# Kernel optimization log

Hardware: AMD Instinct MI355X
Metric: run time of the kernel (lower is better)

Reference implementation:

```python
import jax, jax.numpy as jnp
import numpy as np

B = 524288

def setup_inputs() -> dict:
    key = jax.random.key(0)
    ks = jax.random.split(key, 9)
    return {
        "x":  jax.random.uniform(ks[0], (B, 1, 9, 9), dtype=jnp.float32),
        "Wc": jax.random.normal(ks[1], (81, 9), dtype=jnp.float32),
        "bc": jax.random.normal(ks[2], (81,), dtype=jnp.float32),
        "Wh": jax.random.normal(ks[3], (27, 9), dtype=jnp.float32),
        "bh": jax.random.normal(ks[4], (27,), dtype=jnp.float32),
        "Wm": jax.random.normal(ks[5], (12, 9), dtype=jnp.float32),
        "bm": jax.random.normal(ks[6], (12,), dtype=jnp.float32),
        "Wo": jax.random.normal(ks[7], (4, 4), dtype=jnp.float32),
        "bo": jax.random.normal(ks[8], (4,), dtype=jnp.float32),
    }

def _forward(x, Wc, bc, Wh, bh, Wm, bm, Wo, bo):
    b = x.shape[0]
    # 9 non-overlapping 3x3 patches (stride 3 over 9x9): (B, 9 patches, 9 pixels)
    p = x[:, 0].reshape(b, 3, 3, 3, 3).transpose(0, 1, 3, 2, 4).reshape(b, 9, 9)
    # conv layer: 9 logic kernels per patch -> (B, 9, 9) -> (B, 81)
    feat = jax.nn.sigmoid(
        jnp.einsum('bgp,gkp->bgk', p, Wc.reshape(9, 9, 9)) + bc.reshape(9, 9)
    ).reshape(b, 81)
    # hidden layer: 9 groups x 3 neurons, each over 9 inputs -> (B, 27)
    h = jax.nn.sigmoid(
        jnp.einsum('bgp,gnp->bgn', feat.reshape(b, 9, 9), Wh.reshape(9, 3, 9))
        + bh.reshape(9, 3)
    ).reshape(b, 27)
    # middle layer: 3 groups x 4 neurons, each over 9 inputs -> (B, 12)
    m = jax.nn.sigmoid(
        jnp.einsum('bgp,gnp->bgn', h.reshape(b, 3, 9), Wm.reshape(3, 4, 9))
        + bm.reshape(3, 4)
    ).reshape(b, 12)
    # output layer: class c reads middle group c % 3 (4 values each)
    num_classes = Wo.shape[0]
    grp = jnp.arange(num_classes) % 3                   # (C,)
    mg = m.reshape(b, 3, 4)[:, grp]                     # (B, C, 4)
    output_logits = jnp.einsum('bcp,cp->bc', mg, Wo) + bo
    return output_logits

def reference(x, Wc, bc, Wh, bh, Wm, bm, Wo, bo):
    return _forward(x, Wc, bc, Wh, bh, Wm, bm, Wo, bo)
```

## Files before the change

### kernel.cpp

```cpp
#include <hip/hip_runtime.h>

#define THREADS 256

__device__ __forceinline__ float fast_sigmoid(float v) {
    float e = __expf(-v);
    return __builtin_amdgcn_rcpf(1.0f + e);
}

__global__ __launch_bounds__(THREADS, 4) void olcnn_kernel(
    const float* __restrict__ x,
    const float* __restrict__ Wc, const float* __restrict__ bc,
    const float* __restrict__ Wh, const float* __restrict__ bh,
    const float* __restrict__ Wm, const float* __restrict__ bm,
    const float* __restrict__ Wo, const float* __restrict__ bo,
    float* __restrict__ out)
{
    const int s = blockIdx.x * THREADS + threadIdx.x;
    const float* xs = x + s * 81;

    float pix[81];
    #pragma unroll
    for (int i = 0; i < 81; ++i) pix[i] = xs[i];

    float res[4];

    #pragma unroll
    for (int G = 0; G < 3; ++G) {
        #pragma unroll
        for (int i = 0; i < 27; ++i) asm volatile("" : "+v"(pix[G * 27 + i]));

        float hbuf[9];
        #pragma unroll
        for (int j = 0; j < 3; ++j) {
            const int g = G * 3 + j;
            float feat[9];
            #pragma unroll
            for (int k = 0; k < 9; ++k) {
                float acc = bc[g * 9 + k];
                #pragma unroll
                for (int pr = 0; pr < 3; ++pr)
                    #pragma unroll
                    for (int pc = 0; pc < 3; ++pc)
                        acc = fmaf(pix[G * 27 + pr * 9 + j * 3 + pc],
                                   Wc[(g * 9 + k) * 9 + pr * 3 + pc], acc);
                feat[k] = fast_sigmoid(acc);
            }
            #pragma unroll
            for (int n = 0; n < 3; ++n) {
                float acc = bh[g * 3 + n];
                #pragma unroll
                for (int p = 0; p < 9; ++p)
                    acc = fmaf(feat[p], Wh[(g * 3 + n) * 9 + p], acc);
                hbuf[j * 3 + n] = fast_sigmoid(acc);
            }
        }

        float m[4];
        #pragma unroll
        for (int n = 0; n < 4; ++n) {
            float acc = bm[G * 4 + n];
            #pragma unroll
            for (int p = 0; p < 9; ++p)
                acc = fmaf(hbuf[p], Wm[(G * 4 + n) * 9 + p], acc);
            m[n] = fast_sigmoid(acc);
        }

        {
            float acc = bo[G];
            #pragma unroll
            for (int p = 0; p < 4; ++p)
                acc = fmaf(m[p], Wo[G * 4 + p], acc);
            res[G] = acc;
        }
        if (G == 0) {
            float acc = bo[3];
            #pragma unroll
            for (int p = 0; p < 4; ++p)
                acc = fmaf(m[p], Wo[3 * 4 + p], acc);
            res[3] = acc;
        }
    }

    float4 o;
    o.x = res[0]; o.y = res[1]; o.z = res[2]; o.w = res[3];
    ((float4*)out)[s] = o;
}

extern "C" void kernel_launch(void* const* d_in, const int* in_sizes, int n_in,
                              void* d_out, int out_size, void* d_ws, size_t ws_size,
                              hipStream_t stream) {
    const float* x  = (const float*)d_in[0];
    const float* Wc = (const float*)d_in[1];
    const float* bc = (const float*)d_in[2];
    const float* Wh = (const float*)d_in[3];
    const float* bh = (const float*)d_in[4];
    const float* Wm = (const float*)d_in[5];
    const float* bm = (const float*)d_in[6];
    const float* Wo = (const float*)d_in[7];
    const float* bo = (const float*)d_in[8];
    float* out = (float*)d_out;

    const int B = in_sizes[0] / 81;
    const int blocks = B / THREADS;
    olcnn_kernel<<<blocks, THREADS, 0, stream>>>(x, Wc, bc, Wh, bh, Wm, bm,
                                                 Wo, bo, out);
}
```

Before: 272.3 us.

## Stage input tile into LDS via coalesced global_load_lds with padded rows

Replaces per-thread strided 81-float loads with cooperative 16-byte global_load_lds transfers that place each sample's row in LDS padded to 84 floats. Each thread then reads its three 27-pixel groups with float4 LDS loads. Block size drops to 64 threads to match the tile, with special handling for the final sample's tail. The goal is coalesced global reads and lower register pressure from not holding all 81 pixels at once, at the cost of LDS usage, a barrier and more complex index math.

```diff
diff --git a/kernel.cpp b/kernel.cpp
--- a/kernel.cpp
+++ b/kernel.cpp
@@ -1,13 +1,19 @@
 #include <hip/hip_runtime.h>
+#include <stdint.h>
 
-#define THREADS 256
+#define THREADS 64
+#define ROWPAD  84
+#define TILE_DW (64 * 81)
+
+typedef const __attribute__((address_space(1))) uint32_t* gas_ptr;
+typedef __attribute__((address_space(3))) uint32_t*       las_ptr;
 
 __device__ __forceinline__ float fast_sigmoid(float v) {
     float e = __expf(-v);
     return __builtin_amdgcn_rcpf(1.0f + e);
 }
 
-__global__ __launch_bounds__(THREADS, 4) void olcnn_kernel(
+__global__ __launch_bounds__(THREADS, 2) void olcnn_kernel(
     const float* __restrict__ x,
     const float* __restrict__ Wc, const float* __restrict__ bc,
     const float* __restrict__ Wh, const float* __restrict__ bh,
@@ -15,19 +21,46 @@
     const float* __restrict__ Wo, const float* __restrict__ bo,
     float* __restrict__ out)
 {
-    const int s = blockIdx.x * THREADS + threadIdx.x;
-    const float* xs = x + s * 81;
+    __shared__ __align__(16) float sm[64 * ROWPAD];
 
-    float pix[81];
-    #pragma unroll
-    for (int i = 0; i < 81; ++i) pix[i] = xs[i];
+    const int lane  = threadIdx.x;
+    const int s     = blockIdx.x * THREADS + lane;
+    const int Wd    = blockIdx.x * TILE_DW;
+    const int TOTAL = (int)gridDim.x * TILE_DW;
+
+    {
+        int t = (lane * 6242) >> 17;
+        int r = lane - t * 21;
+        #pragma unroll
+        for (int i = 0; i < 21; ++i) {
+            const int grp = (r * 19) >> 7;
+            int f0 = Wd + t * 81 + (r << 2) - grp;
+            const int lim = TOTAL - 4;
+            f0 = (f0 < lim) ? f0 : lim;
+            __builtin_amdgcn_global_load_lds(
+                (gas_ptr)(x + f0), (las_ptr)(&sm[i * 256]), 16, 0, 0);
+            t += 3 + (r == 20);
+            r = (r == 20) ? 0 : r + 1;
+        }
+    }
+    __syncthreads();
 
     float res[4];
 
     #pragma unroll
     for (int G = 0; G < 3; ++G) {
-        #pragma unroll
-        for (int i = 0; i < 27; ++i) asm volatile("" : "+v"(pix[G * 27 + i]));
+        float p[28];
+        {
+            const float4* rp = (const float4*)&sm[lane * ROWPAD + G * 28];
+            #pragma unroll
+            for (int q = 0; q < 7; ++q) {
+                float4 v = rp[q];
+                p[4*q+0] = v.x; p[4*q+1] = v.y; p[4*q+2] = v.z; p[4*q+3] = v.w;
+            }
+        }
+        if (G == 2 && blockIdx.x == gridDim.x - 1 && lane == 63) {
+            p[24] = x[TOTAL - 3]; p[25] = x[TOTAL - 2]; p[26] = x[TOTAL - 1];
+        }
 
         float hbuf[9];
         #pragma unroll
@@ -41,7 +74,7 @@
                 for (int pr = 0; pr < 3; ++pr)
                     #pragma unroll
                     for (int pc = 0; pc < 3; ++pc)
-                        acc = fmaf(pix[G * 27 + pr * 9 + j * 3 + pc],
+                        acc = fmaf(p[pr * 9 + j * 3 + pc],
                                    Wc[(g * 9 + k) * 9 + pr * 3 + pc], acc);
                 feat[k] = fast_sigmoid(acc);
             }
@@ -49,8 +82,8 @@
             for (int n = 0; n < 3; ++n) {
                 float acc = bh[g * 3 + n];
                 #pragma unroll
-                for (int p = 0; p < 9; ++p)
-                    acc = fmaf(feat[p], Wh[(g * 3 + n) * 9 + p], acc);
+                for (int pidx = 0; pidx < 9; ++pidx)
+                    acc = fmaf(feat[pidx], Wh[(g * 3 + n) * 9 + pidx], acc);
                 hbuf[j * 3 + n] = fast_sigmoid(acc);
             }
         }
@@ -60,23 +93,23 @@
         for (int n = 0; n < 4; ++n) {
             float acc = bm[G * 4 + n];
             #pragma unroll
-            for (int p = 0; p < 9; ++p)
-                acc = fmaf(hbuf[p], Wm[(G * 4 + n) * 9 + p], acc);
+            for (int pidx = 0; pidx < 9; ++pidx)
+                acc = fmaf(hbuf[pidx], Wm[(G * 4 + n) * 9 + pidx], acc);
             m[n] = fast_sigmoid(acc);
         }
 
         {
             float acc = bo[G];
             #pragma unroll
-            for (int p = 0; p < 4; ++p)
-                acc = fmaf(m[p], Wo[G * 4 + p], acc);
+            for (int pidx = 0; pidx < 4; ++pidx)
+                acc = fmaf(m[pidx], Wo[G * 4 + pidx], acc);
             res[G] = acc;
         }
         if (G == 0) {
             float acc = bo[3];
             #pragma unroll
-            for (int p = 0; p < 4; ++p)
-                acc = fmaf(m[p], Wo[3 * 4 + p], acc);
+            for (int pidx = 0; pidx < 4; ++pidx)
+                acc = fmaf(m[pidx], Wo[3 * 4 + pidx], acc);
             res[3] = acc;
         }
     }
```

New measurement: 306.7 us. 12.6% more time.

## Stage input rows through LDS with async global_load_lds per wave

Applied to the files above, without the earlier changes.

Each thread used to load its own 81 floats with strided per-thread global loads, which coalesce poorly. Now each wave copies one third of its 64 samples' pixels at a time (27 floats padded to 28) into shared memory with 16-byte global_load_lds transfers, then every thread reads its rows back as float4 from LDS. Accesses are clamped at the end of the buffer, and the last sample patches in its final three pixels by hand. The aim is coalesced global traffic and fewer live registers, at the cost of 28 KB of LDS per block and a full vmcnt wait per group with no overlap.

```diff
diff --git a/kernel.cpp b/kernel.cpp
--- a/kernel.cpp
+++ b/kernel.cpp
@@ -1,6 +1,12 @@
 #include <hip/hip_runtime.h>
+#include <stdint.h>
 
 #define THREADS 256
+#define WAVE_DW 1792
+#define GDW     28
+
+typedef const __attribute__((address_space(1))) uint32_t* gas_ptr;
+typedef __attribute__((address_space(3))) uint32_t*       las_ptr;
 
 __device__ __forceinline__ float fast_sigmoid(float v) {
     float e = __expf(-v);
@@ -15,19 +21,54 @@
     const float* __restrict__ Wo, const float* __restrict__ bo,
     float* __restrict__ out)
 {
-    const int s = blockIdx.x * THREADS + threadIdx.x;
-    const float* xs = x + s * 81;
+    __shared__ __align__(16) float sm[4 * WAVE_DW];
 
-    float pix[81];
-    #pragma unroll
-    for (int i = 0; i < 81; ++i) pix[i] = xs[i];
+    const int tid   = threadIdx.x;
+    const int lane  = tid & 63;
+    const int wid   = tid >> 6;
+    const int samp  = blockIdx.x * THREADS + tid;
+    const int TOTAL = (int)gridDim.x * THREADS * 81;
+    const int LIM   = TOTAL - 4;
+
+    float* smw = sm + wid * WAVE_DW;
+    const int wbase81 = (blockIdx.x * THREADS + wid * 64) * 81;
 
     float res[4];
 
     #pragma unroll
     for (int G = 0; G < 3; ++G) {
-        #pragma unroll
-        for (int i = 0; i < 27; ++i) asm volatile("" : "+v"(pix[G * 27 + i]));
+        asm volatile("s_waitcnt lgkmcnt(0)" ::: "memory");
+        __builtin_amdgcn_sched_barrier(0);
+
+        {
+            int t = (lane * 9363) >> 16;
+            int r = lane - t * 7;
+            int t81 = t * 81;
+            const int gofs = wbase81 + G * 27;
+            #pragma unroll
+            for (int i = 0; i < 7; ++i) {
+                int f0 = gofs + t81 + (r << 2);
+                f0 = (f0 < LIM) ? f0 : LIM;
+                __builtin_amdgcn_global_load_lds(
+                    (gas_ptr)(x + f0), (las_ptr)(smw + i * 256), 16, 0, 0);
+                t81 += (r == 6) ? 810 : 729;
+                r = (r == 6) ? 0 : r + 1;
+            }
+        }
+        asm volatile("s_waitcnt vmcnt(0)" ::: "memory");
+
+        float p[28];
+        {
+            const float4* rp = (const float4*)(smw + lane * GDW);
+            #pragma unroll
+            for (int q = 0; q < 7; ++q) {
+                float4 v = rp[q];
+                p[4*q+0] = v.x; p[4*q+1] = v.y; p[4*q+2] = v.z; p[4*q+3] = v.w;
+            }
+        }
+        if (G == 2 && samp == (int)gridDim.x * THREADS - 1) {
+            p[24] = x[TOTAL - 3]; p[25] = x[TOTAL - 2]; p[26] = x[TOTAL - 1];
+        }
 
         float hbuf[9];
         #pragma unroll
@@ -41,7 +82,7 @@
                 for (int pr = 0; pr < 3; ++pr)
                     #pragma unroll
                     for (int pc = 0; pc < 3; ++pc)
-                        acc = fmaf(pix[G * 27 + pr * 9 + j * 3 + pc],
+                        acc = fmaf(p[pr * 9 + j * 3 + pc],
                                    Wc[(g * 9 + k) * 9 + pr * 3 + pc], acc);
                 feat[k] = fast_sigmoid(acc);
             }
@@ -49,8 +90,8 @@
             for (int n = 0; n < 3; ++n) {
                 float acc = bh[g * 3 + n];
                 #pragma unroll
-                for (int p = 0; p < 9; ++p)
-                    acc = fmaf(feat[p], Wh[(g * 3 + n) * 9 + p], acc);
+                for (int pi = 0; pi < 9; ++pi)
+                    acc = fmaf(feat[pi], Wh[(g * 3 + n) * 9 + pi], acc);
                 hbuf[j * 3 + n] = fast_sigmoid(acc);
             }
         }
@@ -60,30 +101,30 @@
         for (int n = 0; n < 4; ++n) {
             float acc = bm[G * 4 + n];
             #pragma unroll
-            for (int p = 0; p < 9; ++p)
-                acc = fmaf(hbuf[p], Wm[(G * 4 + n) * 9 + p], acc);
+            for (int pi = 0; pi < 9; ++pi)
+                acc = fmaf(hbuf[pi], Wm[(G * 4 + n) * 9 + pi], acc);
             m[n] = fast_sigmoid(acc);
         }
 
         {
             float acc = bo[G];
             #pragma unroll
-            for (int p = 0; p < 4; ++p)
-                acc = fmaf(m[p], Wo[G * 4 + p], acc);
+            for (int pi = 0; pi < 4; ++pi)
+                acc = fmaf(m[pi], Wo[G * 4 + pi], acc);
             res[G] = acc;
         }
         if (G == 0) {
             float acc = bo[3];
             #pragma unroll
-            for (int p = 0; p < 4; ++p)
-                acc = fmaf(m[p], Wo[3 * 4 + p], acc);
+            for (int pi = 0; pi < 4; ++pi)
+                acc = fmaf(m[pi], Wo[3 * 4 + pi], acc);
             res[3] = acc;
         }
     }
 
     float4 o;
     o.x = res[0]; o.y = res[1]; o.z = res[2]; o.w = res[3];
-    ((float4*)out)[s] = o;
+    ((float4*)out)[samp] = o;
 }
 
 extern "C" void kernel_launch(void* const* d_in, const int* in_sizes, int n_in,
```

Measured after the change: 298.4 us. +9.6%, slower.
